# Kernel optimization log

Hardware: AMD Instinct MI355X
Metric: run time of the kernel (lower is better)

The kernel has to match this reference:

```python
import jax, jax.numpy as jnp
import numpy as np

N_NODES = 100000
D_IN, D_OUT = 1024, 512
B, K = 8192, 64


def setup_inputs() -> dict:
    key = jax.random.key(0)
    k1, k2, k3, k4, k5 = jax.random.split(key, 5)
    X = jax.random.normal(k1, (N_NODES, D_IN), dtype=jnp.float32)
    indices = jax.random.randint(k2, (B, K), 0, N_NODES)  # top-K PPR neighbor ids per batch node
    values = jax.random.uniform(k3, (B, K), dtype=jnp.float32)  # PPR weights
    W = jax.random.normal(k4, (D_IN, D_OUT), dtype=jnp.float32) / np.sqrt(D_IN)
    b = jax.random.normal(k5, (D_OUT,), dtype=jnp.float32)
    return {"X": X, "indices": indices, "values": values, "W": W, "b": b}


def reference(X, indices, values, W, b):
    # Sparse PPR branch. Original: encode only unique gathered rows, then
    # re-expand via inverse indices. Since the encoder is row-pointwise,
    # encoder(X[u_fwd])[u_bwd] == encoder(X)[indices]; we encode all nodes once
    # (n_nodes < B*K here) then gather -- identical math, jit-friendly.
    enc = X @ W + b                      # [N, d_out]
    gathered = enc[indices]              # [B, K, d_out]
    return jnp.einsum('bk,bkd->bd', values, gathered)  # weighted sum over K neighbors
```

## Files before the change

kernel.cpp:

```cpp
#include <hip/hip_runtime.h>

typedef unsigned short ushort_t;
typedef __bf16 bf16x8 __attribute__((ext_vector_type(8)));
typedef float f32x4 __attribute__((ext_vector_type(4)));

#define N_NODES 100000
#define M_PAD   100096
#define D_IN    1024
#define D_OUT   512
#define B_SZ    8192
#define K_NB    64

__device__ __forceinline__ ushort_t f2bf(float f) {
    unsigned int u = __builtin_bit_cast(unsigned int, f);
    u += 0x7FFFu + ((u >> 16) & 1u);
    return (ushort_t)(u >> 16);
}
__device__ __forceinline__ float bflo(unsigned d) {
    return __builtin_bit_cast(float, d << 16);
}
__device__ __forceinline__ float bfhi(unsigned d) {
    return __builtin_bit_cast(float, d & 0xFFFF0000u);
}

__device__ __forceinline__ void gload16(const ushort_t* g, ushort_t* l) {
    __builtin_amdgcn_global_load_lds(
        (const __attribute__((address_space(1))) void*)g,
        (__attribute__((address_space(3))) void*)l,
        16, 0, 0);
}

__device__ __forceinline__ bf16x8 pack8(float4 a, float4 b) {
    bf16x8 r;
    r[0] = (__bf16)a.x; r[1] = (__bf16)a.y;
    r[2] = (__bf16)a.z; r[3] = (__bf16)a.w;
    r[4] = (__bf16)b.x; r[5] = (__bf16)b.y;
    r[6] = (__bf16)b.z; r[7] = (__bf16)b.w;
    return r;
}

__global__ __launch_bounds__(256) void cast_w_kernel(
        const float* __restrict__ W, ushort_t* __restrict__ Wt) {
    int o = blockIdx.x * 256 + threadIdx.x;
    int n = o >> 10;
    int k = o & 1023;
    Wt[o] = f2bf(W[k * D_OUT + n]);
}

__global__ __launch_bounds__(256) void encode_gemm_kernel(
        const float* __restrict__ X, const ushort_t* __restrict__ Wt,
        const float* __restrict__ bias, ushort_t* __restrict__ Enc) {
    int bid = blockIdx.x;
    int logical = (bid & 7) * 391 + (bid >> 3);
    int m0 = (logical >> 2) * 128;
    int n0 = (logical & 3) * 128;

    int t = threadIdx.x;
    int lane = t & 63;
    int wave = t >> 6;
    int wm = (wave >> 1) * 64;
    int wn = (wave & 1) * 64;
    int quad = lane >> 4;
    int l16  = lane & 15;

    __shared__ __align__(16) ushort_t As[128 * 32];
    __shared__ __align__(16) ushort_t Bs[128 * 32];

    f32x4 acc[4][4];
    f32x4 zero = {0.f, 0.f, 0.f, 0.f};
    #pragma unroll
    for (int i = 0; i < 4; i++)
        #pragma unroll
        for (int j = 0; j < 4; j++)
            acc[i][j] = zero;

    int srow = t >> 2;
    int kch  = t & 3;
    int schk = kch ^ ((srow >> 2) & 3);

    const ushort_t* gb = Wt + (size_t)(n0 + srow) * D_IN + schk * 8;
    ushort_t* lb = Bs + t * 8;
    const size_t rowskip = (size_t)64 * D_IN;

    int ar0 = m0 + srow;
    int ar1 = m0 + srow + 64;
    if (ar0 > N_NODES - 1) ar0 = N_NODES - 1;
    if (ar1 > N_NODES - 1) ar1 = N_NODES - 1;
    const float* pa0 = X + (size_t)ar0 * D_IN + kch * 8;
    const float* pa1 = X + (size_t)ar1 * D_IN + kch * 8;
    ushort_t* aw0 = As + srow * 32 + schk * 8;
    ushort_t* aw1 = aw0 + 64 * 32;

    float4 f00 = *(const float4*)(pa0);
    float4 f01 = *(const float4*)(pa0 + 4);
    float4 f10 = *(const float4*)(pa1);
    float4 f11 = *(const float4*)(pa1 + 4);

    int rsw  = (l16 >> 2) & 3;
    int rchk = quad ^ rsw;

    for (int k0 = 0; k0 < D_IN; k0 += 32) {
        *(bf16x8*)aw0 = pack8(f00, f01);
        *(bf16x8*)aw1 = pack8(f10, f11);
        gload16(gb + k0,           lb);
        gload16(gb + rowskip + k0, lb + 2048);
        __syncthreads();

        if (k0 + 32 < D_IN) {
            f00 = *(const float4*)(pa0 + k0 + 32);
            f01 = *(const float4*)(pa0 + k0 + 36);
            f10 = *(const float4*)(pa1 + k0 + 32);
            f11 = *(const float4*)(pa1 + k0 + 36);
        }

        bf16x8 a[4], b[4];
        #pragma unroll
        for (int i = 0; i < 4; i++) {
            a[i] = *(const bf16x8*)(As + (wm + i * 16 + l16) * 32 + rchk * 8);
            b[i] = *(const bf16x8*)(Bs + (wn + i * 16 + l16) * 32 + rchk * 8);
        }
        #pragma unroll
        for (int i = 0; i < 4; i++)
            #pragma unroll
            for (int j = 0; j < 4; j++)
                acc[i][j] = __builtin_amdgcn_mfma_f32_16x16x32_bf16(
                                a[i], b[j], acc[i][j], 0, 0, 0);
        __syncthreads();
    }

    float bv[4];
    #pragma unroll
    for (int j = 0; j < 4; j++) bv[j] = bias[n0 + wn + j * 16 + l16];

    #pragma unroll
    for (int i = 0; i < 4; i++) {
        #pragma unroll
        for (int r = 0; r < 4; r++) {
            int grow = m0 + wm + i * 16 + quad * 4 + r;
            if (grow < N_NODES) {
                #pragma unroll
                for (int j = 0; j < 4; j++) {
                    int gcol = n0 + wn + j * 16 + l16;
                    Enc[(size_t)grow * D_OUT + gcol] = f2bf(acc[i][j][r] + bv[j]);
                }
            }
        }
    }
}

__global__ __launch_bounds__(256) void gather_out_kernel(
        const ushort_t* __restrict__ Enc, const int* __restrict__ idx,
        const float* __restrict__ val, float* __restrict__ out) {
    int b = blockIdx.x;
    int t = threadIdx.x;

    __shared__ int   sidx[K_NB];
    __shared__ float sval[K_NB];
    __shared__ float part[8 * 3 * 64];
    if (t < K_NB) {
        sidx[t] = idx[b * K_NB + t];
        sval[t] = val[b * K_NB + t];
    }
    __syncthreads();

    int h = t >> 6;
    int c = t & 63;

    float acc[8] = {0.f, 0.f, 0.f, 0.f, 0.f, 0.f, 0.f, 0.f};

    uint4 x[8];
    #pragma unroll
    for (int u = 0; u < 8; u++)
        x[u] = ((const uint4*)(Enc + (size_t)sidx[h + 4 * u] * D_OUT))[c];

    #pragma unroll
    for (int j0 = 0; j0 < 16; j0 += 8) {
        uint4 cur[8];
        #pragma unroll
        for (int u = 0; u < 8; u++) cur[u] = x[u];
        if (j0 + 8 < 16) {
            #pragma unroll
            for (int u = 0; u < 8; u++)
                x[u] = ((const uint4*)(
                    Enc + (size_t)sidx[h + 4 * (j0 + 8 + u)] * D_OUT))[c];
        }
        #pragma unroll
        for (int u = 0; u < 8; u++) {
            float v = sval[h + 4 * (j0 + u)];
            acc[0] = fmaf(v, bflo(cur[u].x), acc[0]);
            acc[1] = fmaf(v, bfhi(cur[u].x), acc[1]);
            acc[2] = fmaf(v, bflo(cur[u].y), acc[2]);
            acc[3] = fmaf(v, bfhi(cur[u].y), acc[3]);
            acc[4] = fmaf(v, bflo(cur[u].z), acc[4]);
            acc[5] = fmaf(v, bfhi(cur[u].z), acc[5]);
            acc[6] = fmaf(v, bflo(cur[u].w), acc[6]);
            acc[7] = fmaf(v, bfhi(cur[u].w), acc[7]);
        }
    }

    if (h != 0) {
        #pragma unroll
        for (int e = 0; e < 8; e++)
            part[e * 192 + (h - 1) * 64 + c] = acc[e];
    }
    __syncthreads();
    if (h == 0) {
        float r[8];
        #pragma unroll
        for (int e = 0; e < 8; e++)
            r[e] = acc[e] + part[e * 192 + c] + part[e * 192 + 64 + c]
                          + part[e * 192 + 128 + c];
        float4 o0 = {r[0], r[1], r[2], r[3]};
        float4 o1 = {r[4], r[5], r[6], r[7]};
        float* dst = out + (size_t)b * D_OUT + c * 8;
        *(float4*)(dst)     = o0;
        *(float4*)(dst + 4) = o1;
    }
}

__global__ __launch_bounds__(256) void gather_f32_kernel(
        const float* __restrict__ X, const int* __restrict__ idx,
        const float* __restrict__ val, ushort_t* __restrict__ Y,
        float* __restrict__ s) {
    int b = blockIdx.x;
    int t = threadIdx.x;

    __shared__ int   sidx[K_NB];
    __shared__ float sval[K_NB];
    if (t < K_NB) {
        sidx[t] = idx[b * K_NB + t];
        sval[t] = val[b * K_NB + t];
    }
    __syncthreads();

    float ax = 0.f, ay = 0.f, az = 0.f, aw = 0.f;
    #pragma unroll 8
    for (int k = 0; k < K_NB; k++) {
        const float4* row = (const float4*)(X + (size_t)sidx[k] * D_IN);
        float4 x = row[t];
        float  v = sval[k];
        ax = fmaf(v, x.x, ax);
        ay = fmaf(v, x.y, ay);
        az = fmaf(v, x.z, az);
        aw = fmaf(v, x.w, aw);
    }
    uint2 o;
    o.x = (unsigned)f2bf(ax) | ((unsigned)f2bf(ay) << 16);
    o.y = (unsigned)f2bf(az) | ((unsigned)f2bf(aw) << 16);
    *(uint2*)(Y + (size_t)b * D_IN + t * 4) = o;

    if (t == 0) {
        float sum = 0.f;
        #pragma unroll
        for (int k = 0; k < K_NB; k++) sum += sval[k];
        s[b] = sum;
    }
}

__global__ __launch_bounds__(256) void gemm_kernel(
        const ushort_t* __restrict__ Y, const ushort_t* __restrict__ Wt,
        const float* __restrict__ s, const float* __restrict__ bias,
        float* __restrict__ out) {
    const int Kdim = D_IN;
    int m0 = blockIdx.x * 128;
    int n0 = blockIdx.y * 128;
    int t = threadIdx.x;
    int lane = t & 63;
    int wave = t >> 6;
    int wm = (wave >> 1) * 64;
    int wn = (wave & 1) * 64;
    int quad = lane >> 4;
    int l16  = lane & 15;

    __shared__ __align__(16) ushort_t As[128 * 32];
    __shared__ __align__(16) ushort_t Bs[128 * 32];

    f32x4 acc[4][4];
    f32x4 zero = {0.f, 0.f, 0.f, 0.f};
    #pragma unroll
    for (int i = 0; i < 4; i++)
        #pragma unroll
        for (int j = 0; j < 4; j++)
            acc[i][j] = zero;

    int rsw = (l16 >> 2) & 3;

    for (int k0 = 0; k0 < Kdim; k0 += 32) {
        #pragma unroll
        for (int i = 0; i < 2; i++) {
            int c   = t + i * 256;
            int row = c >> 2;
            int chk = c & 3;
            int pos = chk ^ ((row >> 2) & 3);
            *(int4*)(As + row * 32 + pos * 8) =
                *(const int4*)(Y + (size_t)(m0 + row) * Kdim + k0 + chk * 8);
            *(int4*)(Bs + row * 32 + pos * 8) =
                *(const int4*)(Wt + (size_t)(n0 + row) * Kdim + k0 + chk * 8);
        }
        __syncthreads();

        bf16x8 a[4], b[4];
        int rchk = quad ^ rsw;
        #pragma unroll
        for (int i = 0; i < 4; i++) {
            a[i] = *(const bf16x8*)(As + (wm + i * 16 + l16) * 32 + rchk * 8);
            b[i] = *(const bf16x8*)(Bs + (wn + i * 16 + l16) * 32 + rchk * 8);
        }
        #pragma unroll
        for (int i = 0; i < 4; i++)
            #pragma unroll
            for (int j = 0; j < 4; j++)
                acc[i][j] = __builtin_amdgcn_mfma_f32_16x16x32_bf16(
                                a[i], b[j], acc[i][j], 0, 0, 0);
        __syncthreads();
    }

    #pragma unroll
    for (int i = 0; i < 4; i++) {
        #pragma unroll
        for (int r = 0; r < 4; r++) {
            int grow = m0 + wm + i * 16 + quad * 4 + r;
            float sv = s[grow];
            #pragma unroll
            for (int j = 0; j < 4; j++) {
                int gcol = n0 + wn + j * 16 + l16;
                out[(size_t)grow * D_OUT + gcol] = acc[i][j][r] + sv * bias[gcol];
            }
        }
    }
}

extern "C" void kernel_launch(void* const* d_in, const int* in_sizes, int n_in,
                              void* d_out, int out_size, void* d_ws, size_t ws_size,
                              hipStream_t stream) {
    const float* X    = (const float*)d_in[0];
    const int*   idx  = (const int*)d_in[1];
    const float* val  = (const float*)d_in[2];
    const float* W    = (const float*)d_in[3];
    const float* bias = (const float*)d_in[4];
    float* out = (float*)d_out;

    const size_t ENC_BYTES = (size_t)M_PAD * D_OUT * 2;
    const size_t WT_BYTES  = (size_t)D_OUT * D_IN * 2;
    const size_t Y_BYTES   = (size_t)B_SZ * D_IN * 2;

    char* ws = (char*)d_ws;
    bool fast = ws_size >= ENC_BYTES + WT_BYTES;

    if (fast) {
        ushort_t* Enc = (ushort_t*)ws;
        ushort_t* Wt  = (ushort_t*)(ws + ENC_BYTES);

        hipLaunchKernelGGL(cast_w_kernel, dim3((D_OUT * D_IN) / 256), dim3(256),
                           0, stream, W, Wt);
        hipLaunchKernelGGL(encode_gemm_kernel, dim3((M_PAD / 128) * (D_OUT / 128)),
                           dim3(256), 0, stream, X, Wt, bias, Enc);
        hipLaunchKernelGGL(gather_out_kernel, dim3(B_SZ), dim3(256),
                           0, stream, Enc, idx, val, out);
    } else {
        ushort_t* Yb = (ushort_t*)ws;
        ushort_t* Wt = (ushort_t*)(ws + Y_BYTES);
        float*    sb = (float*)(ws + Y_BYTES + WT_BYTES);

        hipLaunchKernelGGL(cast_w_kernel, dim3((D_OUT * D_IN) / 256), dim3(256),
                           0, stream, W, Wt);
        hipLaunchKernelGGL(gather_f32_kernel, dim3(B_SZ), dim3(256),
                           0, stream, X, idx, val, Yb, sb);
        hipLaunchKernelGGL(gemm_kernel, dim3(B_SZ / 128, D_OUT / 128), dim3(256),
                           0, stream, Yb, Wt, sb, bias, out);
    }
}
```

Baseline: 730.1 us.

## Double-buffer shared-memory tiles in encode GEMM to overlap loads with MFMA

Converts the encode GEMM main loop to a ping-pong scheme over two shared-memory buffers for A and B. Each iteration issues the global loads for the next K-slice into the other buffer, runs the MFMAs on the current one, then writes the converted A data, so only one barrier per iteration remains. The intent is to hide global-load latency behind compute. In exchange it doubles LDS use per block, which may reduce occupancy, and keeps more registers live for the prefetched X values.

```diff
diff --git a/kernel.cpp b/kernel.cpp
--- a/kernel.cpp
+++ b/kernel.cpp
@@ -55,16 +55,16 @@
     int m0 = (logical >> 2) * 128;
     int n0 = (logical & 3) * 128;
 
-    int t = threadIdx.x;
-    int lane = t & 63;
-    int wave = t >> 6;
+    int tid = threadIdx.x;
+    int lane = tid & 63;
+    int wave = tid >> 6;
     int wm = (wave >> 1) * 64;
     int wn = (wave & 1) * 64;
     int quad = lane >> 4;
     int l16  = lane & 15;
 
-    __shared__ __align__(16) ushort_t As[128 * 32];
-    __shared__ __align__(16) ushort_t Bs[128 * 32];
+    __shared__ __align__(16) ushort_t As[2 * 4096];
+    __shared__ __align__(16) ushort_t Bs[2 * 4096];
 
     f32x4 acc[4][4];
     f32x4 zero = {0.f, 0.f, 0.f, 0.f};
@@ -74,12 +74,12 @@
         for (int j = 0; j < 4; j++)
             acc[i][j] = zero;
 
-    int srow = t >> 2;
-    int kch  = t & 3;
+    int srow = tid >> 2;
+    int kch  = tid & 3;
     int schk = kch ^ ((srow >> 2) & 3);
 
     const ushort_t* gb = Wt + (size_t)(n0 + srow) * D_IN + schk * 8;
-    ushort_t* lb = Bs + t * 8;
+    ushort_t* lb = Bs + tid * 8;
     const size_t rowskip = (size_t)64 * D_IN;
 
     int ar0 = m0 + srow;
@@ -88,36 +88,44 @@
     if (ar1 > N_NODES - 1) ar1 = N_NODES - 1;
     const float* pa0 = X + (size_t)ar0 * D_IN + kch * 8;
     const float* pa1 = X + (size_t)ar1 * D_IN + kch * 8;
-    ushort_t* aw0 = As + srow * 32 + schk * 8;
-    ushort_t* aw1 = aw0 + 64 * 32;
-
-    float4 f00 = *(const float4*)(pa0);
-    float4 f01 = *(const float4*)(pa0 + 4);
-    float4 f10 = *(const float4*)(pa1);
-    float4 f11 = *(const float4*)(pa1 + 4);
+    ushort_t* aw = As + srow * 32 + schk * 8;
 
     int rsw  = (l16 >> 2) & 3;
     int rchk = quad ^ rsw;
 
-    for (int k0 = 0; k0 < D_IN; k0 += 32) {
-        *(bf16x8*)aw0 = pack8(f00, f01);
-        *(bf16x8*)aw1 = pack8(f10, f11);
-        gload16(gb + k0,           lb);
-        gload16(gb + rowskip + k0, lb + 2048);
-        __syncthreads();
-
-        if (k0 + 32 < D_IN) {
-            f00 = *(const float4*)(pa0 + k0 + 32);
-            f01 = *(const float4*)(pa0 + k0 + 36);
-            f10 = *(const float4*)(pa1 + k0 + 32);
-            f11 = *(const float4*)(pa1 + k0 + 36);
+    {
+        float4 f00 = *(const float4*)(pa0);
+        float4 f01 = *(const float4*)(pa0 + 4);
+        float4 f10 = *(const float4*)(pa1);
+        float4 f11 = *(const float4*)(pa1 + 4);
+        gload16(gb,           lb);
+        gload16(gb + rowskip, lb + 2048);
+        *(bf16x8*)(aw)           = pack8(f00, f01);
+        *(bf16x8*)(aw + 64 * 32) = pack8(f10, f11);
+    }
+    __syncthreads();
+
+    for (int it = 0; it < 32; ++it) {
+        int p  = (it & 1) * 4096;
+        int q  = 4096 - p;
+        int k1 = it * 32 + 32;
+
+        float4 g00, g01, g10, g11;
+        bool has_next = (k1 < D_IN);
+        if (has_next) {
+            g00 = *(const float4*)(pa0 + k1);
+            g01 = *(const float4*)(pa0 + k1 + 4);
+            g10 = *(const float4*)(pa1 + k1);
+            g11 = *(const float4*)(pa1 + k1 + 4);
+            gload16(gb + k1,           lb + q);
+            gload16(gb + rowskip + k1, lb + q + 2048);
         }
 
         bf16x8 a[4], b[4];
         #pragma unroll
         for (int i = 0; i < 4; i++) {
-            a[i] = *(const bf16x8*)(As + (wm + i * 16 + l16) * 32 + rchk * 8);
-            b[i] = *(const bf16x8*)(Bs + (wn + i * 16 + l16) * 32 + rchk * 8);
+            a[i] = *(const bf16x8*)(As + p + (wm + i * 16 + l16) * 32 + rchk * 8);
+            b[i] = *(const bf16x8*)(Bs + p + (wn + i * 16 + l16) * 32 + rchk * 8);
         }
         #pragma unroll
         for (int i = 0; i < 4; i++)
@@ -125,6 +133,11 @@
             for (int j = 0; j < 4; j++)
                 acc[i][j] = __builtin_amdgcn_mfma_f32_16x16x32_bf16(
                                 a[i], b[j], acc[i][j], 0, 0, 0);
+
+        if (has_next) {
+            *(bf16x8*)(aw + q)           = pack8(g00, g01);
+            *(bf16x8*)(aw + q + 64 * 32) = pack8(g10, g11);
+        }
         __syncthreads();
     }
 
```

New measurement: 783.9 us. +7.4%, slower.
